# Kernel optimization log

Measured on AMD Instinct MI355X. Metric: run time of the kernel, lower is better.

## Reference

```python
import jax, jax.numpy as jnp
import numpy as np

B, C, H, W = 2, 256, 64, 64
KEEP = 0.1


def setup_inputs() -> dict:
    key = jax.random.key(0)
    ks = jax.random.split(key, 7)
    s = 0.05  # small init for 1x1-conv weights
    return {
        "x": jax.random.normal(ks[0], (B, C, H, W), dtype=jnp.float32),
        "Wq": jax.random.normal(ks[1], (C, C), dtype=jnp.float32) * s,
        "bq": jax.random.normal(ks[2], (C,), dtype=jnp.float32) * s,
        "Wk": jax.random.normal(ks[3], (C, C), dtype=jnp.float32) * s,
        "bk": jax.random.normal(ks[4], (C,), dtype=jnp.float32) * s,
        "Wv": jax.random.normal(ks[5], (C, C), dtype=jnp.float32) * s,
        "bv": jax.random.normal(ks[6], (C,), dtype=jnp.float32) * s,
    }


def reference(x, Wq, bq, Wk, bk, Wv, bv):
    b, c, h, w = x.shape
    n = h * w

    def proj(Wm, bm):
        # 1x1 conv == per-pixel linear; output as [B, N, C] tokens
        return jnp.einsum('bchw,oc->bhwo', x, Wm).reshape(b, n, c) + bm

    q = proj(Wq, bq)
    k = proj(Wk, bk)
    v = proj(Wv, bv)

    scores = jnp.einsum('bnc,bmc->bnm', q, k) / (c ** 0.5)  # [B, N, N]
    k_keep = max(1, int(KEEP * n))

    vals, idx = jax.lax.top_k(scores, k_keep)  # [B, N, k_keep]
    # softmax over -inf-masked scores == softmax over topk vals scattered into zeros
    probs = jax.nn.softmax(vals, axis=-1)
    attn = jnp.zeros_like(scores).at[
        jnp.arange(b)[:, None, None], jnp.arange(n)[None, :, None], idx
    ].set(probs)

    out = jnp.einsum('bnm,bmc->bnc', attn, v)  # [B, N, C]
    return out.transpose(0, 2, 1).reshape(b, c, h, w)
```

## Files before the change

kernel.cpp:

```cpp
#include <hip/hip_runtime.h>
#include <hip/hip_bf16.h>
#include <math.h>

#define BATCH 2
#define CC    256
#define NN    4096
#define KK    409
#define KCAT  768
#define SCALE 0.0625f
#define PSTRIDE 4096

typedef _Float16 half8 __attribute__((ext_vector_type(8)));
typedef float    floatx4 __attribute__((ext_vector_type(4)));

typedef __attribute__((address_space(3))) unsigned       lds_u32;
typedef __attribute__((address_space(1))) const unsigned glb_u32;
__device__ __forceinline__ void gload16(const void* g, void* l) {
    __builtin_amdgcn_global_load_lds((glb_u32*)g, (lds_u32*)l, 16, 0, 0);
}

__device__ __forceinline__ unsigned fkey(float f) {
    unsigned u = __float_as_uint(f);
    return (u & 0x80000000u) ? ~u : (u | 0x80000000u);
}
__device__ __forceinline__ float keyToF(unsigned k) {
    unsigned u = (k & 0x80000000u) ? (k ^ 0x80000000u) : ~k;
    return __uint_as_float(u);
}

__global__ __launch_bounds__(256) void xpose_wcat_kernel(
        const float* __restrict__ x,
        const float* __restrict__ Wq, const float* __restrict__ Wk,
        const float* __restrict__ Wv,
        _Float16* __restrict__ xcat, _Float16* __restrict__ Wcat) {
    const int t  = threadIdx.x;
    if (blockIdx.y == 4) {
        int idx = (blockIdx.z * 64 + blockIdx.x) * 256 + t;
#pragma unroll
        for (int k = 0; k < 6; k++) {
            int e = idx + k * 32768;
            int mat = e >> 16;
            int o   = (e >> 8) & 255;
            int c   = e & 255;
            const float* W = (mat == 0) ? Wq : (mat == 1) ? Wk : Wv;
            float v = W[o * 256 + c];
            _Float16 hi = (_Float16)v;
            _Float16 lo = (_Float16)(v - (float)hi);
            _Float16* wr = Wcat + ((size_t)(mat * 256 + o)) * KCAT;
            wr[c] = hi; wr[256 + c] = hi; wr[512 + c] = lo;
        }
        return;
    }

    __shared__ float xs[64][68];
    const int n0 = blockIdx.x * 64;
    const int c0 = blockIdx.y * 64;
    const int b  = blockIdx.z;

    {
        const int ci = t >> 2;
        const int j  = (t & 3) * 16;
        const float* xp = x + ((size_t)((b << 8) + c0 + ci)) * NN + n0 + j;
        float4 a0 = ((const float4*)xp)[0];
        float4 a1 = ((const float4*)xp)[1];
        float4 a2 = ((const float4*)xp)[2];
        float4 a3 = ((const float4*)xp)[3];
        *(float4*)&xs[ci][j]      = a0;
        *(float4*)&xs[ci][j + 4]  = a1;
        *(float4*)&xs[ci][j + 8]  = a2;
        *(float4*)&xs[ci][j + 12] = a3;
    }
    __syncthreads();

    const int n = t >> 2;
    const int g0 = t & 3;
    _Float16* xr = xcat + ((size_t)(b * NN + n0 + n)) * KCAT + c0;
#pragma unroll
    for (int gg = 0; gg < 2; gg++) {
        int g = g0 + gg * 4;
        half8 hi, lo;
#pragma unroll
        for (int k = 0; k < 8; k++) {
            float v = xs[g * 8 + k][n];
            _Float16 h = (_Float16)v;
            hi[k] = h;
            lo[k] = (_Float16)(v - (float)h);
        }
        *(half8*)(xr + g * 8)       = hi;
        *(half8*)(xr + 256 + g * 8) = lo;
        *(half8*)(xr + 512 + g * 8) = hi;
    }
}

__global__ __launch_bounds__(256) void proj_gemm(
        const _Float16* __restrict__ xcat, const _Float16* __restrict__ Wcat,
        const float* __restrict__ bq, const float* __restrict__ bk,
        const float* __restrict__ bv,
        _Float16* __restrict__ Qcat, _Float16* __restrict__ Kcat,
        _Float16* __restrict__ Vt) {
    __shared__ _Float16 As[2][128][64];
    __shared__ _Float16 Bs[2][128][64];

    const int t    = threadIdx.x;
    const int wave = t >> 6;
    const int l    = t & 63;
    const int wr   = wave >> 1;
    const int wc   = wave & 1;
    const int mat  = blockIdx.z;

    int bym, bxn;
    if (mat < 2) { bym = blockIdx.x >> 1; bxn = blockIdx.x & 1; }
    else         { bym = blockIdx.x & 1;  bxn = blockIdx.x >> 1; }

    const int lr = l >> 3;
    const int gg = (l & 7) ^ lr;

    const _Float16* At;
    const _Float16* Bt;
    if (mat < 2) {
        At = xcat + ((size_t)(bym * 128)) * KCAT;
        Bt = Wcat + ((size_t)(mat * 256 + bxn * 128)) * KCAT;
    } else {
        At = Wcat + ((size_t)(512 + bym * 128)) * KCAT;
        Bt = xcat + ((size_t)(bxn * 128)) * KCAT;
    }
    const size_t lane_off = (size_t)lr * KCAT + gg * 8;

    floatx4 acc[4][4];
#pragma unroll
    for (int i = 0; i < 4; i++)
#pragma unroll
        for (int j = 0; j < 4; j++) acc[i][j] = (floatx4)0.0f;

    const int rowA = l & 15;
    const int sg0  = (l >> 4) ^ (l & 7);
    const int sg1  = sg0 ^ 4;

#pragma unroll
    for (int s = 0; s < 4; s++) {
        const int seg = wave * 4 + s;
        gload16(At + (size_t)seg * 8 * KCAT + lane_off, &As[0][seg * 8][0]);
        gload16(Bt + (size_t)seg * 8 * KCAT + lane_off, &Bs[0][seg * 8][0]);
    }
    __syncthreads();

    for (int kt = 0; kt < 12; ++kt) {
        const int cur = kt & 1;
        if (kt < 11) {
            const int kc = (kt + 1) * 64;
#pragma unroll
            for (int s = 0; s < 4; s++) {
                const int seg = wave * 4 + s;
                gload16(At + (size_t)seg * 8 * KCAT + lane_off + kc,
                        &As[cur ^ 1][seg * 8][0]);
                gload16(Bt + (size_t)seg * 8 * KCAT + lane_off + kc,
                        &Bs[cur ^ 1][seg * 8][0]);
            }
        }
#pragma unroll
        for (int ks = 0; ks < 2; ks++) {
            const int sg = ks ? sg1 : sg0;
            half8 af[4], bf[4];
#pragma unroll
            for (int mi = 0; mi < 4; mi++)
                af[mi] = *(const half8*)&As[cur][wr * 64 + mi * 16 + rowA][sg * 8];
#pragma unroll
            for (int ni = 0; ni < 4; ni++)
                bf[ni] = *(const half8*)&Bs[cur][wc * 64 + ni * 16 + rowA][sg * 8];
#pragma unroll
            for (int mi = 0; mi < 4; mi++)
#pragma unroll
                for (int ni = 0; ni < 4; ni++)
                    acc[mi][ni] = __builtin_amdgcn_mfma_f32_16x16x32_f16(
                        af[mi], bf[ni], acc[mi][ni], 0, 0, 0);
        }
        __syncthreads();
    }

    if (mat < 2) {
        const float* bias = (mat == 0) ? bq : bk;
        _Float16* Out = (mat == 0) ? Qcat : Kcat;
#pragma unroll
        for (int ni = 0; ni < 4; ni++) {
            int ch = bxn * 128 + wc * 64 + ni * 16 + (l & 15);
            float bb = bias[ch];
#pragma unroll
            for (int mi = 0; mi < 4; mi++)
#pragma unroll
                for (int rg = 0; rg < 4; rg++) {
                    int token = bym * 128 + wr * 64 + mi * 16 + (l >> 4) * 4 + rg;
                    float v = acc[mi][ni][rg] + bb;
                    _Float16 hi = (_Float16)v;
                    _Float16 lo = (_Float16)(v - (float)hi);
                    _Float16* p = Out + (size_t)token * KCAT + ch;
                    if (mat == 0) { p[0] = hi; p[256] = lo; p[512] = hi; }
                    else          { p[0] = hi; p[256] = hi; p[512] = lo; }
                }
        }
    } else {
#pragma unroll
        for (int mi = 0; mi < 4; mi++)
#pragma unroll
            for (int rg = 0; rg < 4; rg++) {
                int ch = bym * 128 + wr * 64 + mi * 16 + (l >> 4) * 4 + rg;
                float bb = bv[ch];
#pragma unroll
                for (int ni = 0; ni < 4; ni++) {
                    int col = bxn * 128 + wc * 64 + ni * 16 + (l & 15);
                    int b = col >> 12, n = col & 4095;
                    Vt[((size_t)((b << 8) + ch)) * NN + n] =
                        (_Float16)(acc[mi][ni][rg] + bb);
                }
            }
    }
}

__global__ __launch_bounds__(512, 2) void score_gemm(
        const _Float16* __restrict__ Qcat, const _Float16* __restrict__ Kcat,
        _Float16* __restrict__ S) {
    __shared__ _Float16 As[256][64];
    __shared__ _Float16 Bs[256][64];

    const int t    = threadIdx.x;
    const int wave = t >> 6;
    const int l    = t & 63;
    const int wr   = wave >> 1;
    const int wc   = wave & 1;

    const int id  = blockIdx.x;
    const int sc  = id & 7;
    const int j   = id >> 3;
    const int b   = sc & 1;
    const int scq = sc >> 1;
    const int bxn = ((scq & 1) << 3) + (j & 7);
    const int bym = ((scq >> 1) << 3) + (j >> 3);

    const int lr = l >> 3;
    const int gg = (l & 7) ^ lr;

    const _Float16* At = Qcat + ((size_t)((b << 12) + bym * 256)) * KCAT;
    const _Float16* Bt = Kcat + ((size_t)((b << 12) + bxn * 256)) * KCAT;
    const size_t lane_off = (size_t)lr * KCAT + gg * 8;

    floatx4 acc[4][8];
#pragma unroll
    for (int i = 0; i < 4; i++)
#pragma unroll
        for (int jj = 0; jj < 8; jj++) acc[i][jj] = (floatx4)0.0f;

    const int rowA = l & 15;
    const int sg0  = (l >> 4) ^ (l & 7);
    const int sg1  = sg0 ^ 4;

    for (int kc = 0; kc < KCAT; kc += 64) {
#pragma unroll
        for (int s = 0; s < 4; s++) {
            const int seg = wave * 4 + s;
            gload16(At + (size_t)seg * 8 * KCAT + lane_off + kc, &As[seg * 8][0]);
            gload16(Bt + (size_t)seg * 8 * KCAT + lane_off + kc, &Bs[seg * 8][0]);
        }
        __syncthreads();
#pragma unroll
        for (int ks = 0; ks < 2; ks++) {
            const int sg = ks ? sg1 : sg0;
            half8 af[4], bf[8];
#pragma unroll
            for (int mi = 0; mi < 4; mi++)
                af[mi] = *(const half8*)&As[wr * 64 + mi * 16 + rowA][sg * 8];
#pragma unroll
            for (int ni = 0; ni < 8; ni++)
                bf[ni] = *(const half8*)&Bs[wc * 128 + ni * 16 + rowA][sg * 8];
#pragma unroll
            for (int mi = 0; mi < 4; mi++)
#pragma unroll
                for (int ni = 0; ni < 8; ni++)
                    acc[mi][ni] = __builtin_amdgcn_mfma_f32_16x16x32_f16(
                        af[mi], bf[ni], acc[mi][ni], 0, 0, 0);
        }
        __syncthreads();
    }

    _Float16* Sb = S + ((size_t)b << 24);
#pragma unroll
    for (int mi = 0; mi < 4; mi++)
#pragma unroll
        for (int ni = 0; ni < 8; ni++) {
            int col = bxn * 256 + wc * 128 + ni * 16 + (l & 15);
#pragma unroll
            for (int rg = 0; rg < 4; rg++) {
                int row = bym * 256 + wr * 64 + mi * 16 + (l >> 4) * 4 + rg;
                Sb[((size_t)row << 12) + col] =
                    (_Float16)(acc[mi][ni][rg] * SCALE);
            }
        }
}

__global__ __launch_bounds__(256) void select_scatter(
        const _Float16* __restrict__ S, _Float16* __restrict__ P) {
    __shared__ unsigned hist[256];
    __shared__ unsigned scan[256];
    __shared__ unsigned candKey[NN];
    __shared__ unsigned wred[4];
    __shared__ float    fmn[4], fmx[4], wsum[4];
    __shared__ unsigned sh_d, sh_cntgt, sh_T;
    __shared__ int      sh_ncand, sh_need;

    const int t = threadIdx.x;
    const int l = t & 63;
    const int w = t >> 6;

    float    val[16];
    unsigned ukey[16];
    {
        const _Float16* Srow = S + ((size_t)blockIdx.x << 12);
        half8 h0 = *(const half8*)(Srow + t * 16);
        half8 h1 = *(const half8*)(Srow + t * 16 + 8);
#pragma unroll
        for (int jj = 0; jj < 8; jj++) {
            val[jj]     = (float)h0[jj];
            val[jj + 8] = (float)h1[jj];
        }
#pragma unroll
        for (int j = 0; j < 16; j++) ukey[j] = fkey(val[j]);
    }

    float lmin = val[0], lmax = val[0];
#pragma unroll
    for (int j = 1; j < 16; j++) {
        lmin = fminf(lmin, val[j]); lmax = fmaxf(lmax, val[j]);
    }
#pragma unroll
    for (int off = 32; off > 0; off >>= 1) {
        float a = __shfl_down(lmin, off);
        float b = __shfl_down(lmax, off);
        if (l + off < 64) { lmin = fminf(lmin, a); lmax = fmaxf(lmax, b); }
    }
    if (l == 0) { fmn[w] = lmin; fmx[w] = lmax; }

    hist[t] = 0u;
    if (t == 0) sh_ncand = 0;
    __syncthreads();
    const float fmin = fminf(fminf(fmn[0], fmn[1]), fminf(fmn[2], fmn[3]));
    const float fmax = fmaxf(fmaxf(fmx[0], fmx[1]), fmaxf(fmx[2], fmx[3]));
    const float range = fmax - fmin;
    const float bscale = (range > 1e-20f) ? 255.0f / range : 0.0f;

    auto binOf = [&](float v) -> int {
        int bin = (int)((v - fmin) * bscale);
        return bin < 0 ? 0 : (bin > 255 ? 255 : bin);
    };

#pragma unroll
    for (int j = 0; j < 16; j++) atomicAdd(&hist[binOf(val[j])], 1u);
    __syncthreads();

    int rem = KK;

    auto find_digit = [&](int remv) {
        unsigned v = hist[t];
#pragma unroll
        for (int off = 1; off < 64; off <<= 1) {
            unsigned o = __shfl_down(v, off);
            if (l + off < 64) v += o;
        }
        if (l == 0) wred[w] = v;
        __syncthreads();
        unsigned add = 0u;
#pragma unroll
        for (int w2 = 0; w2 < 4; w2++) if (w2 > w) add += wred[w2];
        scan[t] = v + add;
        __syncthreads();
        unsigned sufd  = scan[t];
        unsigned sufd1 = (t < 255) ? scan[t + 1] : 0u;
        if (sufd >= (unsigned)remv && sufd1 < (unsigned)remv) {
            sh_d = (unsigned)t; sh_cntgt = sufd1;
        }
        __syncthreads();
    };

    find_digit(rem);
    const int dbin = (int)sh_d;
    rem -= (int)sh_cntgt;

#pragma unroll
    for (int j = 0; j < 16; j++) {
        if (binOf(val[j]) == dbin) {
            int slot = atomicAdd(&sh_ncand, 1);
            candKey[slot] = ukey[j];
        }
    }
    __syncthreads();
    const int nc = sh_ncand;

    if (nc <= 64) {
        if (w == 0) {
            unsigned kl = (l < nc) ? candKey[l] : 0u;
            int r = 0, g = 0;
            for (int j = 0; j < 64; j++) {
                unsigned kj = __shfl(kl, j);
                bool gt = kj > kl;
                g += gt ? 1 : 0;
                r += (gt || (kj == kl && j < l)) ? 1 : 0;
            }
            if (r == rem - 1) { sh_T = kl; sh_need = rem - g; }
        }
    } else {
        unsigned prefix = 0u;
        int rem2 = rem;
        for (int pass = 0; pass < 4; pass++) {
            const int shift = 24 - 8 * pass;
            hist[t] = 0u;
            __syncthreads();
            for (int i = t; i < nc; i += 256) {
                unsigned u2 = candKey[i];
                if (pass == 0 || (u2 >> (shift + 8)) == (prefix >> (shift + 8)))
                    atomicAdd(&hist[(u2 >> shift) & 255u], 1u);
            }
            __syncthreads();
            find_digit(rem2);
            prefix |= (sh_d << shift);
            rem2 -= (int)sh_cntgt;
        }
        if (t == 0) { sh_T = prefix; sh_need = rem2; }
    }
    __syncthreads();
    const unsigned T = sh_T;
    const int need = sh_need;
    const float mT = keyToF(T);

    int eqc = 0;
#pragma unroll
    for (int j = 0; j < 16; j++) if (ukey[j] == T) eqc++;
    int vinc = eqc;
#pragma unroll
    for (int off = 1; off < 64; off <<= 1) {
        int o = __shfl_up(vinc, off);
        if (l >= off) vinc += o;
    }
    if (l == 63) wred[w] = (unsigned)vinc;
    __syncthreads();
    int addlow = 0;
#pragma unroll
    for (int w2 = 0; w2 < 4; w2++) if (w2 < w) addlow += (int)wred[w2];
    const int eqexcl = vinc - eqc + addlow;

    float pv[16];
    float le = 0.f;
#pragma unroll
    for (int j = 0; j < 16; j++) {
        float e = 0.f;
        if (ukey[j] > T) { e = __expf(val[j] - mT); le += e; }
        pv[j] = e;
    }
    if (eqc) {
        int seen = 0;
#pragma unroll
        for (int j = 0; j < 16; j++) {
            if (ukey[j] == T) {
                if (eqexcl + seen < need) { pv[j] = 1.0f; le += 1.0f; }
                seen++;
            }
        }
    }

#pragma unroll
    for (int off = 32; off > 0; off >>= 1) {
        float o = __shfl_down(le, off);
        if (l + off < 64) le += o;
    }
    if (l == 0) wsum[w] = le;
    __syncthreads();
    const float inv = 1.0f / (wsum[0] + wsum[1] + wsum[2] + wsum[3]);

    half8 ra, rb;
#pragma unroll
    for (int j = 0; j < 8; j++) {
        ra[j] = (_Float16)(pv[j] * inv);
        rb[j] = (_Float16)(pv[j + 8] * inv);
    }
    _Float16* Pr = P + (size_t)blockIdx.x * PSTRIDE + t * 16;
    *(half8*)Pr       = ra;
    *(half8*)(Pr + 8) = rb;
}

__global__ __launch_bounds__(256) void av_gemm(
        const _Float16* __restrict__ Vt, const _Float16* __restrict__ P,
        float* __restrict__ out) {
    __shared__ _Float16 As[2][64][64];
    __shared__ _Float16 Bs[2][64][64];

    const int t    = threadIdx.x;
    const int wave = t >> 6;
    const int l    = t & 63;
    const int wr   = wave >> 1;
    const int wc   = wave & 1;
    const int bxn  = blockIdx.x;
    const int byc  = blockIdx.y;
    const int b    = blockIdx.z;

    const int lr = l >> 3;
    const int gg = (l & 7) ^ lr;

    const _Float16* At = Vt + ((size_t)((b << 8) + byc * 64)) * NN;
    const _Float16* Bt = P + ((size_t)(b * NN + bxn * 64)) * PSTRIDE;
    const size_t lane_offA = (size_t)lr * NN + gg * 8;
    const size_t lane_offB = (size_t)lr * PSTRIDE + gg * 8;

    floatx4 acc[2][2];
#pragma unroll
    for (int i = 0; i < 2; i++)
#pragma unroll
        for (int j = 0; j < 2; j++) acc[i][j] = (floatx4)0.0f;

    const int rowA   = l & 15;
    const int sgbase = (l >> 4) ^ (l & 7);

#pragma unroll
    for (int s = 0; s < 2; s++) {
        const int seg = wave * 2 + s;
        gload16(At + (size_t)seg * 8 * NN + lane_offA,      &As[0][seg * 8][0]);
        gload16(Bt + (size_t)seg * 8 * PSTRIDE + lane_offB, &Bs[0][seg * 8][0]);
    }
    __syncthreads();

    for (int kt = 0; kt < 64; ++kt) {
        const int cur = kt & 1;
        if (kt < 63) {
            const int kc = (kt + 1) * 64;
#pragma unroll
            for (int s = 0; s < 2; s++) {
                const int seg = wave * 2 + s;
                gload16(At + (size_t)seg * 8 * NN + lane_offA + kc,
                        &As[cur ^ 1][seg * 8][0]);
                gload16(Bt + (size_t)seg * 8 * PSTRIDE + lane_offB + kc,
                        &Bs[cur ^ 1][seg * 8][0]);
            }
        }
#pragma unroll
        for (int st = 0; st < 2; st++) {
            const int sg = sgbase ^ (st ? 4 : 0);
            half8 af[2], bf[2];
#pragma unroll
            for (int mi = 0; mi < 2; mi++)
                af[mi] = *(const half8*)&As[cur][wr * 32 + mi * 16 + rowA][sg * 8];
#pragma unroll
            for (int ni = 0; ni < 2; ni++)
                bf[ni] = *(const half8*)&Bs[cur][wc * 32 + ni * 16 + rowA][sg * 8];
#pragma unroll
            for (int mi = 0; mi < 2; mi++)
#pragma unroll
                for (int ni = 0; ni < 2; ni++)
                    acc[mi][ni] = __builtin_amdgcn_mfma_f32_16x16x32_f16(
                        af[mi], bf[ni], acc[mi][ni], 0, 0, 0);
        }
        __syncthreads();
    }

#pragma unroll
    for (int mi = 0; mi < 2; mi++)
#pragma unroll
        for (int ni = 0; ni < 2; ni++) {
            int col = bxn * 64 + wc * 32 + ni * 16 + (l & 15);
#pragma unroll
            for (int rg = 0; rg < 4; rg++) {
                int row = byc * 64 + wr * 32 + mi * 16 + (l >> 4) * 4 + rg;
                out[((size_t)((b << 8) + row) << 12) + col] = acc[mi][ni][rg];
            }
        }
}

extern "C" void kernel_launch(void* const* d_in, const int* in_sizes, int n_in,
                              void* d_out, int out_size, void* d_ws, size_t ws_size,
                              hipStream_t stream) {
    const float* x  = (const float*)d_in[0];
    const float* Wq = (const float*)d_in[1];
    const float* bq = (const float*)d_in[2];
    const float* Wk = (const float*)d_in[3];
    const float* bk = (const float*)d_in[4];
    const float* Wv = (const float*)d_in[5];
    const float* bv = (const float*)d_in[6];
    float* out = (float*)d_out;

    char* ws = (char*)d_ws;
    _Float16* Wcat = (_Float16*)ws;
    _Float16* Qcat = (_Float16*)(ws + 1179648);
    _Float16* Kcat = (_Float16*)(ws + 1179648 + 12582912);
    _Float16* Vt   = (_Float16*)(ws + 1179648 + 2 * 12582912);
    _Float16* S    = (_Float16*)(ws + 1179648 + 2 * 12582912 + 4194304);
    _Float16* xcat = (_Float16*)S;
    _Float16* P    = (_Float16*)S;

    xpose_wcat_kernel<<<dim3(64, 5, BATCH), 256, 0, stream>>>(x, Wq, Wk, Wv,
                                                              xcat, Wcat);
    proj_gemm<<<dim3(128, 1, 3), 256, 0, stream>>>(xcat, Wcat, bq, bk, bv,
                                                   Qcat, Kcat, Vt);
    score_gemm<<<dim3(512, 1, 1), 512, 0, stream>>>(Qcat, Kcat, S);
    select_scatter<<<BATCH * NN, 256, 0, stream>>>(S, P);
    av_gemm<<<dim3(64, 4, BATCH), 256, 0, stream>>>(Vt, P, out);
}
```

Baseline: 246.6 us.

## Double-buffer score GEMM LDS tiles with K-step of 32

Splits the score GEMM's shared-memory tiles into two buffers of 32-wide K slices and prefetches the next slice with direct global-to-LDS loads while MFMAs run on the current one. The aim is to hide global load latency that the old load-sync-compute loop exposed. It adds a new swizzle pattern for the narrower tiles and runs twice as many loop iterations, each with a barrier. The single barrier per iteration may not order the overwrite of the buffer being read, which is a race risk.

```diff
diff --git a/kernel.cpp b/kernel.cpp
--- a/kernel.cpp
+++ b/kernel.cpp
@@ -218,8 +218,8 @@
 __global__ __launch_bounds__(512, 2) void score_gemm(
         const _Float16* __restrict__ Qcat, const _Float16* __restrict__ Kcat,
         _Float16* __restrict__ S) {
-    __shared__ _Float16 As[256][64];
-    __shared__ _Float16 Bs[256][64];
+    __shared__ _Float16 As[2][256][32];
+    __shared__ _Float16 Bs[2][256][32];
 
     const int t    = threadIdx.x;
     const int wave = t >> 6;
@@ -235,12 +235,11 @@
     const int bxn = ((scq & 1) << 3) + (j & 7);
     const int bym = ((scq >> 1) << 3) + (j >> 3);
 
-    const int lr = l >> 3;
-    const int gg = (l & 7) ^ lr;
+    const int g = (l & 3) ^ ((l >> 3) & 3);
+    const size_t lane_off = (size_t)(l >> 2) * KCAT + g * 8;
 
     const _Float16* At = Qcat + ((size_t)((b << 12) + bym * 256)) * KCAT;
     const _Float16* Bt = Kcat + ((size_t)((b << 12) + bxn * 256)) * KCAT;
-    const size_t lane_off = (size_t)lr * KCAT + gg * 8;
 
     floatx4 acc[4][8];
 #pragma unroll
@@ -249,34 +248,42 @@
         for (int jj = 0; jj < 8; jj++) acc[i][jj] = (floatx4)0.0f;
 
     const int rowA = l & 15;
-    const int sg0  = (l >> 4) ^ (l & 7);
-    const int sg1  = sg0 ^ 4;
-
-    for (int kc = 0; kc < KCAT; kc += 64) {
-#pragma unroll
-        for (int s = 0; s < 4; s++) {
-            const int seg = wave * 4 + s;
-            gload16(At + (size_t)seg * 8 * KCAT + lane_off + kc, &As[seg * 8][0]);
-            gload16(Bt + (size_t)seg * 8 * KCAT + lane_off + kc, &Bs[seg * 8][0]);
-        }
-        __syncthreads();
-#pragma unroll
-        for (int ks = 0; ks < 2; ks++) {
-            const int sg = ks ? sg1 : sg0;
-            half8 af[4], bf[8];
-#pragma unroll
-            for (int mi = 0; mi < 4; mi++)
-                af[mi] = *(const half8*)&As[wr * 64 + mi * 16 + rowA][sg * 8];
+    const int sgr  = (l >> 4) ^ ((rowA >> 1) & 3);
+
+#pragma unroll
+    for (int s = 0; s < 2; s++) {
+        const int seg = wave * 2 + s;
+        gload16(At + (size_t)seg * 16 * KCAT + lane_off, &As[0][seg * 16][0]);
+        gload16(Bt + (size_t)seg * 16 * KCAT + lane_off, &Bs[0][seg * 16][0]);
+    }
+    __syncthreads();
+
+    for (int kt = 0; kt < 24; ++kt) {
+        const int cur = kt & 1;
+        if (kt < 23) {
+            const int kc = (kt + 1) * 32;
+#pragma unroll
+            for (int s = 0; s < 2; s++) {
+                const int seg = wave * 2 + s;
+                gload16(At + (size_t)seg * 16 * KCAT + lane_off + kc,
+                        &As[cur ^ 1][seg * 16][0]);
+                gload16(Bt + (size_t)seg * 16 * KCAT + lane_off + kc,
+                        &Bs[cur ^ 1][seg * 16][0]);
+            }
+        }
+        half8 af[4], bf[8];
+#pragma unroll
+        for (int mi = 0; mi < 4; mi++)
+            af[mi] = *(const half8*)&As[cur][wr * 64 + mi * 16 + rowA][sgr * 8];
+#pragma unroll
+        for (int ni = 0; ni < 8; ni++)
+            bf[ni] = *(const half8*)&Bs[cur][wc * 128 + ni * 16 + rowA][sgr * 8];
+#pragma unroll
+        for (int mi = 0; mi < 4; mi++)
 #pragma unroll
             for (int ni = 0; ni < 8; ni++)
-                bf[ni] = *(const half8*)&Bs[wc * 128 + ni * 16 + rowA][sg * 8];
-#pragma unroll
-            for (int mi = 0; mi < 4; mi++)
-#pragma unroll
-                for (int ni = 0; ni < 8; ni++)
-                    acc[mi][ni] = __builtin_amdgcn_mfma_f32_16x16x32_f16(
-                        af[mi], bf[ni], acc[mi][ni], 0, 0, 0);
-        }
+                acc[mi][ni] = __builtin_amdgcn_mfma_f32_16x16x32_f16(
+                    af[mi], bf[ni], acc[mi][ni], 0, 0, 0);
         __syncthreads();
     }
 
```

New measurement: 255.0 us. 1.03x slower.
